# Performance work log

Hardware: AMD Instinct MI355X
Metric: run time of the kernel (lower is better)

The kernel has to match this reference:

```python
import jax, jax.numpy as jnp
import numpy as np

N_NODES = 50000
N_EDGES = 800000
F_IN = 512
HID = 256
N_CLS = 40
W_DIM = 50  # dimension*dimension*2 with dimension=5


def _prelu(x, a):
    return jnp.where(x >= 0, x, a * x)


def _segment_softmax(w, idx, n):
    # per-segment (grouped by idx), per-channel numerically stable softmax
    m = jax.ops.segment_max(w, idx, num_segments=n)
    e = jnp.exp(w - m[idx])
    s = jax.ops.segment_sum(e, idx, num_segments=n)
    return e / s[idx]


def _curvgn(x, edge_index, w_mul, W, b, w0, a, w1, b1):
    n = x.shape[0]
    h = x @ W + b                                   # [N, C]
    ow = _prelu(w_mul @ w0, a) @ w1 + b1            # [E, C] edge-weight MLP
    ow = _segment_softmax(ow, edge_index[0], n)     # softmax grouped by source (as in source)
    msg = ow * h[edge_index[0]]                     # gather x_j, weight
    return jax.ops.segment_sum(msg, edge_index[1], num_segments=n)  # scatter-add at target


def setup_inputs() -> dict:
    key = jax.random.key(0)
    ks = jax.random.split(key, 12)
    s = 0.05
    return {
        "x": jax.random.normal(ks[0], (N_NODES, F_IN), jnp.float32),
        "edge_index": jax.random.randint(ks[1], (2, N_EDGES), 0, N_NODES, jnp.int64 if jax.config.jax_enable_x64 else jnp.int32).astype(jnp.int32),
        "w_mul": jax.random.normal(ks[2], (N_EDGES, W_DIM), jnp.float32),
        "W1": jax.random.normal(ks[3], (F_IN, HID), jnp.float32) * s,
        "b1": jnp.zeros((HID,), jnp.float32),
        "m1_w0": jax.random.normal(ks[4], (W_DIM, HID), jnp.float32) * s,
        "m1_a": jnp.full((HID,), 0.2, jnp.float32),
        "m1_w1": jax.random.normal(ks[5], (HID, HID), jnp.float32) * s,
        "m1_b1": jnp.zeros((HID,), jnp.float32),
        "W2": jax.random.normal(ks[6], (HID, N_CLS), jnp.float32) * s,
        "b2": jnp.zeros((N_CLS,), jnp.float32),
        "m2_w0": jax.random.normal(ks[7], (W_DIM, N_CLS), jnp.float32) * s,
        "m2_a": jnp.full((N_CLS,), 0.2, jnp.float32),
        "m2_w1": jax.random.normal(ks[8], (N_CLS, N_CLS), jnp.float32) * s,
        "m2_b1": jnp.zeros((N_CLS,), jnp.float32),
    }


def reference(x, edge_index, w_mul, W1, b1, m1_w0, m1_a, m1_w1, m1_b1,
              W2, b2, m2_w0, m2_a, m2_w1, m2_b1):
    # eval mode: dropout is identity
    h = _curvgn(x, edge_index, w_mul, W1, b1, m1_w0, m1_a, m1_w1, m1_b1)
    h = jax.nn.elu(h)
    out = _curvgn(h, edge_index, w_mul, W2, b2, m2_w0, m2_a, m2_w1, m2_b1)
    return jax.nn.log_softmax(out, axis=1)
```

## Files before the change

### kernel.cpp

```cpp
#include <hip/hip_runtime.h>
#include <hip/hip_bf16.h>
#include <math.h>

#define N_NODESC 50000
#define N_EDGESC 800000
#define F_INC 512
#define HIDC 256
#define N_CLSC 40
#define W_DIMC 50
#define HN (2*N_NODESC)
#define NB_SCAN 196

typedef __bf16 bf16;
typedef __bf16 bf16x8 __attribute__((ext_vector_type(8)));
typedef __bf16 bf16x4 __attribute__((ext_vector_type(4)));
typedef __bf16 bf16x2 __attribute__((ext_vector_type(2)));
typedef float  f32x4  __attribute__((ext_vector_type(4)));
typedef float  f32x2  __attribute__((ext_vector_type(2)));

__global__ void k_hist(const int* __restrict__ ei, int* __restrict__ hist) {
    int e = blockIdx.x*256 + threadIdx.x;
    if (e < N_EDGESC) {
        atomicAdd(&hist[ei[e]], 1);
        atomicAdd(&hist[N_NODESC + ei[N_EDGESC + e]], 1);
    }
}
__global__ void k_copy(int* d, const int* s, int n) {
    int i = blockIdx.x*256 + threadIdx.x;
    if (i < n) d[i] = s[i];
}
__global__ void k_scan_part(const int* __restrict__ hist, int* __restrict__ part) {
    __shared__ int lds[512];
    int t = threadIdx.x;
    int i = blockIdx.x*512 + t;
    lds[t] = (i < HN) ? hist[i] : 0;
    __syncthreads();
    for (int off = 256; off > 0; off >>= 1) {
        if (t < off) lds[t] += lds[t+off];
        __syncthreads();
    }
    if (t == 0) part[blockIdx.x] = lds[0];
}
__global__ void k_scan_mid(const int* __restrict__ part, int* __restrict__ partx) {
    __shared__ int lds[256];
    int t = threadIdx.x;
    int v = (t < NB_SCAN) ? part[t] : 0;
    lds[t] = v;
    __syncthreads();
    for (int off = 1; off < 256; off <<= 1) {
        int add = (t >= off) ? lds[t-off] : 0;
        __syncthreads();
        lds[t] += add;
        __syncthreads();
    }
    partx[t] = lds[t] - v;
}
__global__ void k_scan_apply(const int* __restrict__ hist, const int* __restrict__ partx,
                             int* __restrict__ basev) {
    __shared__ int lds[512];
    int t = threadIdx.x;
    int i = blockIdx.x*512 + t;
    int v = (i < HN) ? hist[i] : 0;
    lds[t] = v;
    __syncthreads();
    for (int off = 1; off < 512; off <<= 1) {
        int add = (t >= off) ? lds[t-off] : 0;
        __syncthreads();
        lds[t] += add;
        __syncthreads();
    }
    if (i < HN) basev[i] = lds[t] - v + partx[blockIdx.x];
}
__global__ void k_scatter(const int* __restrict__ ei, int* __restrict__ cursor,
                          int* __restrict__ perm_src,
                          int* __restrict__ spd, int* __restrict__ svd) {
    int e = blockIdx.x*256 + threadIdx.x;
    if (e >= N_EDGESC) return;
    int s = ei[e];
    int d = ei[N_EDGESC + e];
    int p = atomicAdd(&cursor[s], 1);
    perm_src[p] = e;
    int q = atomicAdd(&cursor[N_NODESC + d], 1) - N_EDGESC;
    spd[q] = p;
    svd[q] = s;
}

__global__ void k_tconv(const float* __restrict__ src, bf16* __restrict__ dst,
                        int Ks, int Ns, int Kp, int Np) {
    int idx = blockIdx.x*256 + threadIdx.x;
    if (idx >= Kp*Np) return;
    int n = idx / Kp, k = idx - n*Kp;
    float v = (k < Ks && n < Ns) ? src[k*Ns + n] : 0.f;
    dst[idx] = (bf16)v;
}

__global__ __launch_bounds__(256) void k_h1(const float* __restrict__ x,
                                            const bf16* __restrict__ W1t,
                                            const float* __restrict__ b1,
                                            bf16* __restrict__ h1) {
    __shared__ __align__(16) bf16 a_lds[64*40];
    int tid = threadIdx.x;
    int lane = tid & 63, wv = tid >> 6;
    int l15 = lane & 15, quad = lane >> 4;
    int r0 = blockIdx.x * 64;
    f32x4 acc[4][4] = {};
    for (int ks = 0; ks < 16; ++ks) {
        #pragma unroll
        for (int i = 0; i < 2; ++i) {
            int idx = tid + i*256;
            int rl = idx >> 3, c4 = idx & 7;
            int rg = r0 + rl;
            f32x4 v = {};
            if (rg < N_NODESC) v = *(const f32x4*)&x[(size_t)rg*F_INC + ks*32 + c4*4];
            bf16x4 b; b[0]=(bf16)v[0]; b[1]=(bf16)v[1]; b[2]=(bf16)v[2]; b[3]=(bf16)v[3];
            *(bf16x4*)&a_lds[rl*40 + c4*4] = b;
        }
        __syncthreads();
        bf16x8 af[4], bfr[4];
        #pragma unroll
        for (int mt = 0; mt < 4; ++mt)
            af[mt] = *(const bf16x8*)&a_lds[(mt*16 + l15)*40 + quad*8];
        #pragma unroll
        for (int nt = 0; nt < 4; ++nt) {
            int n = wv*64 + nt*16 + l15;
            bfr[nt] = *(const bf16x8*)&W1t[n*F_INC + ks*32 + quad*8];
        }
        #pragma unroll
        for (int mt = 0; mt < 4; ++mt)
            #pragma unroll
            for (int nt = 0; nt < 4; ++nt)
                acc[mt][nt] = __builtin_amdgcn_mfma_f32_16x16x32_bf16(af[mt], bfr[nt], acc[mt][nt], 0, 0, 0);
        __syncthreads();
    }
    #pragma unroll
    for (int nt = 0; nt < 4; ++nt) {
        int col = wv*64 + nt*16 + l15;
        float bias = b1[col];
        #pragma unroll
        for (int mt = 0; mt < 4; ++mt)
            #pragma unroll
            for (int r = 0; r < 4; ++r) {
                int row = r0 + mt*16 + quad*4 + r;
                if (row < N_NODESC) h1[(size_t)row*HIDC + col] = (bf16)(acc[mt][nt][r] + bias);
            }
    }
}

__global__ __launch_bounds__(256) void k_mlp1a(
    const float* __restrict__ w_mul, const int* __restrict__ perm_src,
    const bf16* __restrict__ w0t, const float* __restrict__ a1,
    bf16* __restrict__ u1) {
    __shared__ __align__(16) bf16 wm[64*72];
    __shared__ __align__(16) bf16 bw[256*72];
    __shared__ int e_lds[64];
    int tid = threadIdx.x;
    int lane = tid & 63, wv = tid >> 6;
    int l15 = lane & 15, quad = lane >> 4;
    int p0 = blockIdx.x * 64;

    if (tid < 64) e_lds[tid] = perm_src[p0 + tid];
    #pragma unroll
    for (int i = 0; i < 8; ++i) {
        int idx = i*256 + tid;
        int n = idx >> 3, j = idx & 7;
        *(bf16x8*)&bw[n*72 + j*8] = *(const bf16x8*)&w0t[n*64 + j*8];
    }
    __syncthreads();
    #pragma unroll
    for (int i = 0; i < 7; ++i) {
        int idx = i*256 + tid;
        if (idx < 1600) {
            int row = idx / 25;
            int k = 2*(idx - row*25);
            f32x2 v = *(const f32x2*)&w_mul[(size_t)e_lds[row]*W_DIMC + k];
            bf16x2 b; b[0] = (bf16)v[0]; b[1] = (bf16)v[1];
            *(bf16x2*)&wm[row*72 + k] = b;
        }
    }
    #pragma unroll
    for (int i = 0; i < 2; ++i) {
        int idx = i*256 + tid;
        if (idx < 448) {
            int row = idx / 7, c = 50 + 2*(idx - row*7);
            bf16x2 z; z[0] = (bf16)0.f; z[1] = (bf16)0.f;
            *(bf16x2*)&wm[row*72 + c] = z;
        }
    }
    __syncthreads();

    f32x4 acc[4][4] = {};
    #pragma unroll
    for (int ks = 0; ks < 2; ++ks) {
        bf16x8 af[4], bfr[4];
        #pragma unroll
        for (int mt = 0; mt < 4; ++mt)
            af[mt] = *(const bf16x8*)&wm[(mt*16 + l15)*72 + ks*32 + quad*8];
        #pragma unroll
        for (int i = 0; i < 4; ++i)
            bfr[i] = *(const bf16x8*)&bw[(wv*64 + i*16 + l15)*72 + ks*32 + quad*8];
        #pragma unroll
        for (int mt = 0; mt < 4; ++mt)
            #pragma unroll
            for (int i = 0; i < 4; ++i)
                acc[mt][i] = __builtin_amdgcn_mfma_f32_16x16x32_bf16(af[mt], bfr[i], acc[mt][i], 0, 0, 0);
    }
    #pragma unroll
    for (int i = 0; i < 4; ++i) {
        int col = wv*64 + i*16 + l15;
        float al = a1[col];
        #pragma unroll
        for (int mt = 0; mt < 4; ++mt)
            #pragma unroll
            for (int r = 0; r < 4; ++r) {
                float v = acc[mt][i][r];
                v = (v >= 0.f) ? v : al*v;
                u1[(size_t)(p0 + mt*16 + quad*4 + r)*HIDC + col] = (bf16)v;
            }
    }
}

__global__ __launch_bounds__(256) void k_mlp1b(
    const int* __restrict__ perm_src, const int* __restrict__ ei,
    const bf16* __restrict__ w1t, const float* __restrict__ bb1,
    bf16* __restrict__ eow1,
    float* __restrict__ s1) {
    __shared__ __align__(16) bf16 t1[64*264];
    __shared__ int sv[64];
    int tid = threadIdx.x;
    int lane = tid & 63, wv = tid >> 6;
    int l15 = lane & 15, quad = lane >> 4;
    int p0 = blockIdx.x * 64;

    if (tid < 64) sv[tid] = ei[perm_src[p0 + tid]];
    #pragma unroll
    for (int i = 0; i < 8; ++i) {
        int idx = i*256 + tid;
        int row = idx >> 5, j = idx & 31;
        *(bf16x8*)&t1[row*264 + j*8] = *(const bf16x8*)&eow1[(size_t)(p0 + row)*HIDC + j*8];
    }
    __syncthreads();

    f32x4 acc[4][4] = {};
    #pragma unroll
    for (int ks = 0; ks < 8; ++ks) {
        bf16x8 af[4], bfr[4];
        #pragma unroll
        for (int mt = 0; mt < 4; ++mt)
            af[mt] = *(const bf16x8*)&t1[(mt*16 + l15)*264 + ks*32 + quad*8];
        #pragma unroll
        for (int i = 0; i < 4; ++i)
            bfr[i] = *(const bf16x8*)&w1t[(wv*64 + i*16 + l15)*HIDC + ks*32 + quad*8];
        #pragma unroll
        for (int mt = 0; mt < 4; ++mt)
            #pragma unroll
            for (int i = 0; i < 4; ++i)
                acc[mt][i] = __builtin_amdgcn_mfma_f32_16x16x32_bf16(af[mt], bfr[i], acc[mt][i], 0, 0, 0);
    }
    __syncthreads();
    #pragma unroll
    for (int i = 0; i < 4; ++i) {
        int col = wv*64 + i*16 + l15;
        float bias = bb1[col];
        #pragma unroll
        for (int mt = 0; mt < 4; ++mt)
            #pragma unroll
            for (int r = 0; r < 4; ++r)
                t1[(mt*16 + quad*4 + r)*264 + col] = (bf16)__expf(acc[mt][i][r] + bias);
    }
    __syncthreads();
    #pragma unroll
    for (int i = 0; i < 8; ++i) {
        int idx = i*256 + tid;
        int row = idx >> 5, j = idx & 31;
        *(bf16x8*)&eow1[(size_t)(p0 + row)*HIDC + j*8] = *(const bf16x8*)&t1[row*264 + j*8];
    }
    {
        int c = tid;
        float acc2 = 0.f;
        #pragma unroll
        for (int r = 0; r < 64; ++r) {
            acc2 += (float)t1[r*264 + c];
            if (r == 63 || sv[r+1] != sv[r]) {
                atomicAdd(&s1[(size_t)sv[r]*HIDC + c], acc2);
                acc2 = 0.f;
            }
        }
    }
}

__global__ __launch_bounds__(256) void k_mlp2(
    const float* __restrict__ w_mul, const int* __restrict__ perm_src,
    const int* __restrict__ ei,
    const bf16* __restrict__ w20t, const float* __restrict__ a2,
    const bf16* __restrict__ w21t, const float* __restrict__ bb2,
    bf16* __restrict__ eow2, float* __restrict__ s2) {
    __shared__ __align__(16) bf16 wm[64*72];
    __shared__ __align__(16) bf16 t2[64*72];
    __shared__ int e_lds[64], sv[64];
    int tid = threadIdx.x;
    int lane = tid & 63, wv = tid >> 6;
    int l15 = lane & 15, quad = lane >> 4;
    int p0 = blockIdx.x * 64;

    if (tid < 64) {
        int e = perm_src[p0 + tid];
        e_lds[tid] = e;
        sv[tid] = ei[e];
    }
    __syncthreads();
    #pragma unroll
    for (int i = 0; i < 7; ++i) {
        int idx = i*256 + tid;
        if (idx < 1600) {
            int row = idx / 25;
            int k = 2*(idx - row*25);
            f32x2 v = *(const f32x2*)&w_mul[(size_t)e_lds[row]*W_DIMC + k];
            bf16x2 b; b[0] = (bf16)v[0]; b[1] = (bf16)v[1];
            *(bf16x2*)&wm[row*72 + k] = b;
        }
    }
    #pragma unroll
    for (int i = 0; i < 2; ++i) {
        int idx = i*256 + tid;
        if (idx < 448) {
            int row = idx / 7, c = 50 + 2*(idx - row*7);
            bf16x2 z; z[0] = (bf16)0.f; z[1] = (bf16)0.f;
            *(bf16x2*)&wm[row*72 + c] = z;
        }
    }
    #pragma unroll
    for (int i = 0; i < 2; ++i) {
        int idx = i*256 + tid;
        int row = idx >> 3, c = 48 + 2*(idx & 7);
        bf16x2 z; z[0] = (bf16)0.f; z[1] = (bf16)0.f;
        *(bf16x2*)&t2[row*72 + c] = z;
    }
    __syncthreads();

    {
        f32x4 acc[3] = {};
        #pragma unroll
        for (int ks = 0; ks < 2; ++ks) {
            bf16x8 af = *(const bf16x8*)&wm[(wv*16 + l15)*72 + ks*32 + quad*8];
            #pragma unroll
            for (int i = 0; i < 3; ++i) {
                bf16x8 bfr = *(const bf16x8*)&w20t[(i*16 + l15)*64 + ks*32 + quad*8];
                acc[i] = __builtin_amdgcn_mfma_f32_16x16x32_bf16(af, bfr, acc[i], 0, 0, 0);
            }
        }
        #pragma unroll
        for (int i = 0; i < 3; ++i) {
            int col = i*16 + l15;
            float al = (col < N_CLSC) ? a2[col] : 0.f;
            #pragma unroll
            for (int r = 0; r < 4; ++r) {
                float v = acc[i][r];
                v = (v >= 0.f) ? v : al*v;
                t2[(wv*16 + quad*4 + r)*72 + col] = (bf16)v;
            }
        }
    }
    __syncthreads();
    {
        f32x4 acc[3] = {};
        #pragma unroll
        for (int ks = 0; ks < 2; ++ks) {
            bf16x8 af = *(const bf16x8*)&t2[(wv*16 + l15)*72 + ks*32 + quad*8];
            #pragma unroll
            for (int i = 0; i < 3; ++i) {
                bf16x8 bfr = *(const bf16x8*)&w21t[(i*16 + l15)*64 + ks*32 + quad*8];
                acc[i] = __builtin_amdgcn_mfma_f32_16x16x32_bf16(af, bfr, acc[i], 0, 0, 0);
            }
        }
        __syncthreads();
        #pragma unroll
        for (int i = 0; i < 3; ++i) {
            int col = i*16 + l15;
            if (col < N_CLSC) {
                float bias = bb2[col];
                #pragma unroll
                for (int r = 0; r < 4; ++r)
                    t2[(wv*16 + quad*4 + r)*72 + col] = (bf16)__expf(acc[i][r] + bias);
            }
        }
    }
    __syncthreads();
    #pragma unroll
    for (int i = 0; i < 2; ++i) {
        int idx = i*256 + tid;
        if (idx < 320) {
            int row = idx / 5, c8 = idx % 5;
            bf16x8 v = *(const bf16x8*)&t2[row*72 + c8*8];
            *(bf16x8*)&eow2[(size_t)(p0 + row)*N_CLSC + c8*8] = v;
        }
    }
    if (tid < 240) {
        int c = tid % 40, g = tid / 40;
        int rA = g*11, rB = (rA + 11 < 64) ? rA + 11 : 64;
        float acc = 0.f;
        for (int r = rA; r < rB; ++r) {
            acc += (float)t2[r*72 + c];
            if (r == rB-1 || sv[r+1] != sv[r]) {
                atomicAdd(&s2[(size_t)sv[r]*N_CLSC + c], acc);
                acc = 0.f;
            }
        }
    }
}

__global__ __launch_bounds__(256) void k_agg1(
    const bf16* __restrict__ eow1, const bf16* __restrict__ g1,
    const int* __restrict__ basev, const int* __restrict__ spd,
    const int* __restrict__ svd, float* __restrict__ out1) {
    int v = blockIdx.x, c = threadIdx.x;
    int b = basev[N_NODESC + v] - N_EDGESC;
    int e = (v < N_NODESC-1) ? basev[N_NODESC + v + 1] - N_EDGESC : N_EDGESC;
    float acc = 0.f;
    #pragma unroll 2
    for (int j = b; j < e; ++j) {
        int sp = spd[j], s = svd[j];
        acc += (float)eow1[(size_t)sp*HIDC + c] * (float)g1[(size_t)s*HIDC + c];
    }
    out1[(size_t)v*HIDC + c] = (acc > 0.f) ? acc : expm1f(acc);
}

__global__ __launch_bounds__(64) void k_agg2(
    const bf16* __restrict__ eow2, const bf16* __restrict__ g2,
    const int* __restrict__ basev, const int* __restrict__ spd,
    const int* __restrict__ svd, float* __restrict__ out) {
    int v = blockIdx.x, c = threadIdx.x;
    int b = basev[N_NODESC + v] - N_EDGESC;
    int e = (v < N_NODESC-1) ? basev[N_NODESC + v + 1] - N_EDGESC : N_EDGESC;
    bool act = (c < N_CLSC);
    float acc = 0.f;
    #pragma unroll 2
    for (int j = b; j < e; ++j) {
        int sp = spd[j], s = svd[j];
        if (act) acc += (float)eow2[(size_t)sp*N_CLSC + c] * (float)g2[(size_t)s*N_CLSC + c];
    }
    float m = act ? acc : -INFINITY;
    #pragma unroll
    for (int off = 32; off > 0; off >>= 1) m = fmaxf(m, __shfl_xor(m, off));
    float ex = act ? __expf(acc - m) : 0.f;
    #pragma unroll
    for (int off = 32; off > 0; off >>= 1) ex += __shfl_xor(ex, off);
    if (act) out[(size_t)v*N_CLSC + c] = acc - m - logf(ex);
}

__global__ void k_div_bf4(bf16* __restrict__ h, const float* __restrict__ s, int n4) {
    int i = blockIdx.x*256 + threadIdx.x;
    if (i < n4) {
        bf16x4 hv = *(bf16x4*)&h[i*4];
        f32x4 sv = *(const f32x4*)&s[i*4];
        #pragma unroll
        for (int k = 0; k < 4; ++k) hv[k] = (bf16)((float)hv[k] / sv[k]);
        *(bf16x4*)&h[i*4] = hv;
    }
}
__global__ void k_h2(const float* __restrict__ out1, const float* __restrict__ W2,
                     const float* __restrict__ b2, bf16* __restrict__ h2) {
    int i = blockIdx.x*256 + threadIdx.x;
    if (i >= N_NODESC*N_CLSC) return;
    int v = i / N_CLSC, c = i - v*N_CLSC;
    float acc = b2[c];
    const float* row = &out1[(size_t)v*HIDC];
    #pragma unroll 4
    for (int k = 0; k < HIDC; ++k) acc += row[k] * W2[k*N_CLSC + c];
    h2[i] = (bf16)acc;
}

extern "C" void kernel_launch(void* const* d_in, const int* in_sizes, int n_in,
                              void* d_out, int out_size, void* d_ws, size_t ws_size,
                              hipStream_t stream) {
    const float* x    = (const float*)d_in[0];
    const int*   ei   = (const int*)d_in[1];
    const float* wmul = (const float*)d_in[2];
    const float* W1   = (const float*)d_in[3];
    const float* b1   = (const float*)d_in[4];
    const float* m1w0 = (const float*)d_in[5];
    const float* m1a  = (const float*)d_in[6];
    const float* m1w1 = (const float*)d_in[7];
    const float* m1b1 = (const float*)d_in[8];
    const float* W2   = (const float*)d_in[9];
    const float* b2   = (const float*)d_in[10];
    const float* m2w0 = (const float*)d_in[11];
    const float* m2a  = (const float*)d_in[12];
    const float* m2w1 = (const float*)d_in[13];
    const float* m2b1 = (const float*)d_in[14];
    float* out = (float*)d_out;

    char* ws = (char*)d_ws;
    size_t off = 0;
    auto alloc = [&](size_t bytes) -> void* {
        off = (off + 255) & ~(size_t)255;
        void* p = ws + off;
        off += bytes;
        return p;
    };
    bf16*  h1g1  = (bf16*) alloc((size_t)N_NODESC*HIDC*2);
    float* s1o1  = (float*)alloc((size_t)N_NODESC*HIDC*4);
    bf16*  h2g2  = (bf16*) alloc((size_t)N_NODESC*N_CLSC*2);
    float* s2    = (float*)alloc((size_t)N_NODESC*N_CLSC*4);
    bf16*  W1t   = (bf16*) alloc(256*512*2);
    bf16*  w0t   = (bf16*) alloc(256*64*2);
    bf16*  w1tm  = (bf16*) alloc(256*256*2);
    bf16*  w20t  = (bf16*) alloc(48*64*2);
    bf16*  w21t  = (bf16*) alloc(48*64*2);
    int*   hist  = (int*)  alloc(HN*4);
    int*   basev = (int*)  alloc(HN*4);
    int*   cursor= (int*)  alloc(HN*4);
    int*   part  = (int*)  alloc(256*4);
    int*   partx = (int*)  alloc(256*4);
    int*   perm_src = (int*)alloc((size_t)N_EDGESC*4);
    int*   spd      = (int*)alloc((size_t)N_EDGESC*4);
    int*   svd      = (int*)alloc((size_t)N_EDGESC*4);
    bf16*  eow1  = (bf16*) alloc((size_t)N_EDGESC*HIDC*2);
    bf16*  eow2  = (bf16*) alloc((size_t)N_EDGESC*N_CLSC*2);

    hipMemsetAsync(hist, 0, HN*4, stream);
    hipMemsetAsync(s1o1, 0, (size_t)N_NODESC*HIDC*4, stream);
    hipMemsetAsync(s2,   0, (size_t)N_NODESC*N_CLSC*4, stream);
    k_hist<<<(N_EDGESC+255)/256, 256, 0, stream>>>(ei, hist);
    k_scan_part<<<NB_SCAN, 512, 0, stream>>>(hist, part);
    k_scan_mid<<<1, 256, 0, stream>>>(part, partx);
    k_scan_apply<<<NB_SCAN, 512, 0, stream>>>(hist, partx, basev);
    k_copy<<<(HN+255)/256, 256, 0, stream>>>(cursor, basev, HN);
    k_scatter<<<(N_EDGESC+255)/256, 256, 0, stream>>>(ei, cursor, perm_src, spd, svd);

    k_tconv<<<(512*256+255)/256, 256, 0, stream>>>(W1,   W1t, 512, 256, 512, 256);
    k_tconv<<<(256*64+255)/256,  256, 0, stream>>>(m1w0, w0t,  50, 256,  64, 256);
    k_tconv<<<(256*256+255)/256, 256, 0, stream>>>(m1w1, w1tm, 256, 256, 256, 256);
    k_tconv<<<(48*64+255)/256,   256, 0, stream>>>(m2w0, w20t,  50,  40,  64,  48);
    k_tconv<<<(48*64+255)/256,   256, 0, stream>>>(m2w1, w21t,  40,  40,  64,  48);

    k_h1<<<(N_NODESC+63)/64, 256, 0, stream>>>(x, W1t, b1, h1g1);
    k_mlp1a<<<N_EDGESC/64, 256, 0, stream>>>(wmul, perm_src, w0t, m1a, eow1);
    k_mlp1b<<<N_EDGESC/64, 256, 0, stream>>>(perm_src, ei, w1tm, m1b1, eow1, s1o1);
    k_mlp2<<<N_EDGESC/64, 256, 0, stream>>>(wmul, perm_src, ei, w20t, m2a, w21t, m2b1,
                                            eow2, s2);
    k_div_bf4<<<(N_NODESC*HIDC/4+255)/256, 256, 0, stream>>>(h1g1, s1o1, N_NODESC*HIDC/4);
    k_agg1<<<N_NODESC, 256, 0, stream>>>(eow1, h1g1, basev, spd, svd, s1o1);

    k_h2<<<(N_NODESC*N_CLSC+255)/256, 256, 0, stream>>>(s1o1, W2, b2, h2g2);
    k_div_bf4<<<(N_NODESC*N_CLSC/4+255)/256, 256, 0, stream>>>(h2g2, s2, N_NODESC*N_CLSC/4);
    k_agg2<<<N_NODESC, 64, 0, stream>>>(eow2, h2g2, basev, spd, svd, out);
}
```

Baseline: 1.745 ms.

## Fuse layer-1 edge MLP kernels and double edge tile in layer-2 MLP

Merges the two layer-1 edge-MLP kernels into one, so the PReLU intermediate stays in shared memory rather than being written to and re-read from the global eow1 buffer. The second GEMM now double-buffers its operand fragments across k-steps, and the first reads w0t directly from global memory instead of staging it in LDS. The layer-2 edge MLP handles 128 edges per block, with each wave computing two M-tiles, and one barrier between its stages is dropped. This cuts global traffic and launch count, at the cost of higher register pressure and a different shared-memory footprint and occupancy.

New measurement: 1.501 ms. 14.0% less time.

```diff
diff --git a/kernel.cpp b/kernel.cpp
--- a/kernel.cpp
+++ b/kernel.cpp
@@ -146,24 +146,24 @@
     }
 }
 
-__global__ __launch_bounds__(256) void k_mlp1a(
+__global__ __launch_bounds__(256) void k_mlp1(
     const float* __restrict__ w_mul, const int* __restrict__ perm_src,
+    const int* __restrict__ ei,
     const bf16* __restrict__ w0t, const float* __restrict__ a1,
-    bf16* __restrict__ u1) {
+    const bf16* __restrict__ w1t, const float* __restrict__ bb1,
+    bf16* __restrict__ eow1, float* __restrict__ s1) {
     __shared__ __align__(16) bf16 wm[64*72];
-    __shared__ __align__(16) bf16 bw[256*72];
-    __shared__ int e_lds[64];
+    __shared__ __align__(16) bf16 t1[64*264];
+    __shared__ int e_lds[64], sv[64];
     int tid = threadIdx.x;
     int lane = tid & 63, wv = tid >> 6;
     int l15 = lane & 15, quad = lane >> 4;
     int p0 = blockIdx.x * 64;
 
-    if (tid < 64) e_lds[tid] = perm_src[p0 + tid];
-    #pragma unroll
-    for (int i = 0; i < 8; ++i) {
-        int idx = i*256 + tid;
-        int n = idx >> 3, j = idx & 7;
-        *(bf16x8*)&bw[n*72 + j*8] = *(const bf16x8*)&w0t[n*64 + j*8];
+    if (tid < 64) {
+        int e = perm_src[p0 + tid];
+        e_lds[tid] = e;
+        sv[tid] = ei[e];
     }
     __syncthreads();
     #pragma unroll
@@ -188,86 +188,81 @@
     }
     __syncthreads();
 
-    f32x4 acc[4][4] = {};
-    #pragma unroll
-    for (int ks = 0; ks < 2; ++ks) {
-        bf16x8 af[4], bfr[4];
+    {
+        f32x4 acc[4][4] = {};
+        bf16x8 af[2][4], bfr[2][4];
+        #pragma unroll
+        for (int ks = 0; ks < 2; ++ks) {
+            #pragma unroll
+            for (int mt = 0; mt < 4; ++mt)
+                af[ks][mt] = *(const bf16x8*)&wm[(mt*16 + l15)*72 + ks*32 + quad*8];
+            #pragma unroll
+            for (int i = 0; i < 4; ++i)
+                bfr[ks][i] = *(const bf16x8*)&w0t[(wv*64 + i*16 + l15)*64 + ks*32 + quad*8];
+        }
+        #pragma unroll
+        for (int ks = 0; ks < 2; ++ks)
+            #pragma unroll
+            for (int mt = 0; mt < 4; ++mt)
+                #pragma unroll
+                for (int i = 0; i < 4; ++i)
+                    acc[mt][i] = __builtin_amdgcn_mfma_f32_16x16x32_bf16(af[ks][mt], bfr[ks][i], acc[mt][i], 0, 0, 0);
+        #pragma unroll
+        for (int i = 0; i < 4; ++i) {
+            int col = wv*64 + i*16 + l15;
+            float al = a1[col];
+            #pragma unroll
+            for (int mt = 0; mt < 4; ++mt)
+                #pragma unroll
+                for (int r = 0; r < 4; ++r) {
+                    float v = acc[mt][i][r];
+                    v = (v >= 0.f) ? v : al*v;
+                    t1[(mt*16 + quad*4 + r)*264 + col] = (bf16)v;
+                }
+        }
+    }
+    __syncthreads();
+
+    {
+        f32x4 acc[4][4] = {};
+        bf16x8 af[2][4], bfr[2][4];
         #pragma unroll
         for (int mt = 0; mt < 4; ++mt)
-            af[mt] = *(const bf16x8*)&wm[(mt*16 + l15)*72 + ks*32 + quad*8];
+            af[0][mt] = *(const bf16x8*)&t1[(mt*16 + l15)*264 + quad*8];
         #pragma unroll
         for (int i = 0; i < 4; ++i)
-            bfr[i] = *(const bf16x8*)&bw[(wv*64 + i*16 + l15)*72 + ks*32 + quad*8];
-        #pragma unroll
-        for (int mt = 0; mt < 4; ++mt)
-            #pragma unroll
-            for (int i = 0; i < 4; ++i)
-                acc[mt][i] = __builtin_amdgcn_mfma_f32_16x16x32_bf16(af[mt], bfr[i], acc[mt][i], 0, 0, 0);
-    }
-    #pragma unroll
-    for (int i = 0; i < 4; ++i) {
-        int col = wv*64 + i*16 + l15;
-        float al = a1[col];
-        #pragma unroll
-        for (int mt = 0; mt < 4; ++mt)
-            #pragma unroll
-            for (int r = 0; r < 4; ++r) {
-                float v = acc[mt][i][r];
-                v = (v >= 0.f) ? v : al*v;
-                u1[(size_t)(p0 + mt*16 + quad*4 + r)*HIDC + col] = (bf16)v;
+            bfr[0][i] = *(const bf16x8*)&w1t[(wv*64 + i*16 + l15)*HIDC + quad*8];
+        #pragma unroll
+        for (int ks = 0; ks < 8; ++ks) {
+            int cur = ks & 1, nxt = cur ^ 1;
+            if (ks < 7) {
+                #pragma unroll
+                for (int mt = 0; mt < 4; ++mt)
+                    af[nxt][mt] = *(const bf16x8*)&t1[(mt*16 + l15)*264 + (ks+1)*32 + quad*8];
+                #pragma unroll
+                for (int i = 0; i < 4; ++i)
+                    bfr[nxt][i] = *(const bf16x8*)&w1t[(wv*64 + i*16 + l15)*HIDC + (ks+1)*32 + quad*8];
             }
-    }
-}
-
-__global__ __launch_bounds__(256) void k_mlp1b(
-    const int* __restrict__ perm_src, const int* __restrict__ ei,
-    const bf16* __restrict__ w1t, const float* __restrict__ bb1,
-    bf16* __restrict__ eow1,
-    float* __restrict__ s1) {
-    __shared__ __align__(16) bf16 t1[64*264];
-    __shared__ int sv[64];
-    int tid = threadIdx.x;
-    int lane = tid & 63, wv = tid >> 6;
-    int l15 = lane & 15, quad = lane >> 4;
-    int p0 = blockIdx.x * 64;
-
-    if (tid < 64) sv[tid] = ei[perm_src[p0 + tid]];
-    #pragma unroll
-    for (int i = 0; i < 8; ++i) {
-        int idx = i*256 + tid;
-        int row = idx >> 5, j = idx & 31;
-        *(bf16x8*)&t1[row*264 + j*8] = *(const bf16x8*)&eow1[(size_t)(p0 + row)*HIDC + j*8];
-    }
-    __syncthreads();
-
-    f32x4 acc[4][4] = {};
-    #pragma unroll
-    for (int ks = 0; ks < 8; ++ks) {
-        bf16x8 af[4], bfr[4];
-        #pragma unroll
-        for (int mt = 0; mt < 4; ++mt)
-            af[mt] = *(const bf16x8*)&t1[(mt*16 + l15)*264 + ks*32 + quad*8];
-        #pragma unroll
-        for (int i = 0; i < 4; ++i)
-            bfr[i] = *(const bf16x8*)&w1t[(wv*64 + i*16 + l15)*HIDC + ks*32 + quad*8];
-        #pragma unroll
-        for (int mt = 0; mt < 4; ++mt)
-            #pragma unroll
-            for (int i = 0; i < 4; ++i)
-                acc[mt][i] = __builtin_amdgcn_mfma_f32_16x16x32_bf16(af[mt], bfr[i], acc[mt][i], 0, 0, 0);
-    }
-    __syncthreads();
-    #pragma unroll
-    for (int i = 0; i < 4; ++i) {
-        int col = wv*64 + i*16 + l15;
-        float bias = bb1[col];
-        #pragma unroll
-        for (int mt = 0; mt < 4; ++mt)
-            #pragma unroll
-            for (int r = 0; r < 4; ++r)
-                t1[(mt*16 + quad*4 + r)*264 + col] = (bf16)__expf(acc[mt][i][r] + bias);
-    }
-    __syncthreads();
+            #pragma unroll
+            for (int mt = 0; mt < 4; ++mt)
+                #pragma unroll
+                for (int i = 0; i < 4; ++i)
+                    acc[mt][i] = __builtin_amdgcn_mfma_f32_16x16x32_bf16(af[cur][mt], bfr[cur][i], acc[mt][i], 0, 0, 0);
+        }
+        __syncthreads();
+        #pragma unroll
+        for (int i = 0; i < 4; ++i) {
+            int col = wv*64 + i*16 + l15;
+            float bias = bb1[col];
+            #pragma unroll
+            for (int mt = 0; mt < 4; ++mt)
+                #pragma unroll
+                for (int r = 0; r < 4; ++r)
+                    t1[(mt*16 + quad*4 + r)*264 + col] = (bf16)__expf(acc[mt][i][r] + bias);
+        }
+    }
+    __syncthreads();
+
     #pragma unroll
     for (int i = 0; i < 8; ++i) {
         int idx = i*256 + tid;
@@ -294,24 +289,24 @@
     const bf16* __restrict__ w20t, const float* __restrict__ a2,
     const bf16* __restrict__ w21t, const float* __restrict__ bb2,
     bf16* __restrict__ eow2, float* __restrict__ s2) {
-    __shared__ __align__(16) bf16 wm[64*72];
-    __shared__ __align__(16) bf16 t2[64*72];
-    __shared__ int e_lds[64], sv[64];
+    __shared__ __align__(16) bf16 wm[128*72];
+    __shared__ __align__(16) bf16 t2[128*72];
+    __shared__ int e_lds[128], sv[128];
     int tid = threadIdx.x;
     int lane = tid & 63, wv = tid >> 6;
     int l15 = lane & 15, quad = lane >> 4;
-    int p0 = blockIdx.x * 64;
-
-    if (tid < 64) {
+    int p0 = blockIdx.x * 128;
+
+    if (tid < 128) {
         int e = perm_src[p0 + tid];
         e_lds[tid] = e;
         sv[tid] = ei[e];
     }
     __syncthreads();
     #pragma unroll
-    for (int i = 0; i < 7; ++i) {
-        int idx = i*256 + tid;
-        if (idx < 1600) {
+    for (int i = 0; i < 13; ++i) {
+        int idx = i*256 + tid;
+        if (idx < 3200) {
             int row = idx / 25;
             int k = 2*(idx - row*25);
             f32x2 v = *(const f32x2*)&w_mul[(size_t)e_lds[row]*W_DIMC + k];
@@ -320,16 +315,16 @@
         }
     }
     #pragma unroll
-    for (int i = 0; i < 2; ++i) {
-        int idx = i*256 + tid;
-        if (idx < 448) {
+    for (int i = 0; i < 4; ++i) {
+        int idx = i*256 + tid;
+        if (idx < 896) {
             int row = idx / 7, c = 50 + 2*(idx - row*7);
             bf16x2 z; z[0] = (bf16)0.f; z[1] = (bf16)0.f;
             *(bf16x2*)&wm[row*72 + c] = z;
         }
     }
     #pragma unroll
-    for (int i = 0; i < 2; ++i) {
+    for (int i = 0; i < 4; ++i) {
         int idx = i*256 + tid;
         int row = idx >> 3, c = 48 + 2*(idx & 7);
         bf16x2 z; z[0] = (bf16)0.f; z[1] = (bf16)0.f;
@@ -338,57 +333,73 @@
     __syncthreads();
 
     {
-        f32x4 acc[3] = {};
+        f32x4 acc[2][3] = {};
         #pragma unroll
         for (int ks = 0; ks < 2; ++ks) {
-            bf16x8 af = *(const bf16x8*)&wm[(wv*16 + l15)*72 + ks*32 + quad*8];
-            #pragma unroll
-            for (int i = 0; i < 3; ++i) {
-                bf16x8 bfr = *(const bf16x8*)&w20t[(i*16 + l15)*64 + ks*32 + quad*8];
-                acc[i] = __builtin_amdgcn_mfma_f32_16x16x32_bf16(af, bfr, acc[i], 0, 0, 0);
-            }
+            bf16x8 af[2], bfr[3];
+            #pragma unroll
+            for (int mt = 0; mt < 2; ++mt)
+                af[mt] = *(const bf16x8*)&wm[(wv*32 + mt*16 + l15)*72 + ks*32 + quad*8];
+            #pragma unroll
+            for (int i = 0; i < 3; ++i)
+                bfr[i] = *(const bf16x8*)&w20t[(i*16 + l15)*64 + ks*32 + quad*8];
+            #pragma unroll
+            for (int mt = 0; mt < 2; ++mt)
+                #pragma unroll
+                for (int i = 0; i < 3; ++i)
+                    acc[mt][i] = __builtin_amdgcn_mfma_f32_16x16x32_bf16(af[mt], bfr[i], acc[mt][i], 0, 0, 0);
         }
         #pragma unroll
         for (int i = 0; i < 3; ++i) {
             int col = i*16 + l15;
             float al = (col < N_CLSC) ? a2[col] : 0.f;
             #pragma unroll
-            for (int r = 0; r < 4; ++r) {
-                float v = acc[i][r];
-                v = (v >= 0.f) ? v : al*v;
-                t2[(wv*16 + quad*4 + r)*72 + col] = (bf16)v;
-            }
-        }
-    }
-    __syncthreads();
+            for (int mt = 0; mt < 2; ++mt)
+                #pragma unroll
+                for (int r = 0; r < 4; ++r) {
+                    float v = acc[mt][i][r];
+                    v = (v >= 0.f) ? v : al*v;
+                    t2[(wv*32 + mt*16 + quad*4 + r)*72 + col] = (bf16)v;
+                }
+        }
+    }
+
     {
-        f32x4 acc[3] = {};
+        f32x4 acc[2][3] = {};
         #pragma unroll
         for (int ks = 0; ks < 2; ++ks) {
-            bf16x8 af = *(const bf16x8*)&t2[(wv*16 + l15)*72 + ks*32 + quad*8];
-            #pragma unroll
-            for (int i = 0; i < 3; ++i) {
-                bf16x8 bfr = *(const bf16x8*)&w21t[(i*16 + l15)*64 + ks*32 + quad*8];
-                acc[i] = __builtin_amdgcn_mfma_f32_16x16x32_bf16(af, bfr, acc[i], 0, 0, 0);
-            }
-        }
-        __syncthreads();
+            bf16x8 af[2], bfr[3];
+            #pragma unroll
+            for (int mt = 0; mt < 2; ++mt)
+                af[mt] = *(const bf16x8*)&t2[(wv*32 + mt*16 + l15)*72 + ks*32 + quad*8];
+            #pragma unroll
+            for (int i = 0; i < 3; ++i)
+                bfr[i] = *(const bf16x8*)&w21t[(i*16 + l15)*64 + ks*32 + quad*8];
+            #pragma unroll
+            for (int mt = 0; mt < 2; ++mt)
+                #pragma unroll
+                for (int i = 0; i < 3; ++i)
+                    acc[mt][i] = __builtin_amdgcn_mfma_f32_16x16x32_bf16(af[mt], bfr[i], acc[mt][i], 0, 0, 0);
+        }
         #pragma unroll
         for (int i = 0; i < 3; ++i) {
             int col = i*16 + l15;
             if (col < N_CLSC) {
                 float bias = bb2[col];
                 #pragma unroll
-                for (int r = 0; r < 4; ++r)
-                    t2[(wv*16 + quad*4 + r)*72 + col] = (bf16)__expf(acc[i][r] + bias);
+                for (int mt = 0; mt < 2; ++mt)
+                    #pragma unroll
+                    for (int r = 0; r < 4; ++r)
+                        t2[(wv*32 + mt*16 + quad*4 + r)*72 + col] = (bf16)__expf(acc[mt][i][r] + bias);
             }
         }
     }
     __syncthreads();
-    #pragma unroll
-    for (int i = 0; i < 2; ++i) {
-        int idx = i*256 + tid;
-        if (idx < 320) {
+
+    #pragma unroll
+    for (int i = 0; i < 3; ++i) {
+        int idx = i*256 + tid;
+        if (idx < 640) {
             int row = idx / 5, c8 = idx % 5;
             bf16x8 v = *(const bf16x8*)&t2[row*72 + c8*8];
             *(bf16x8*)&eow2[(size_t)(p0 + row)*N_CLSC + c8*8] = v;
@@ -396,7 +407,7 @@
     }
     if (tid < 240) {
         int c = tid % 40, g = tid / 40;
-        int rA = g*11, rB = (rA + 11 < 64) ? rA + 11 : 64;
+        int rA = g*22, rB = (rA + 22 < 128) ? rA + 22 : 128;
         float acc = 0.f;
         for (int r = rA; r < rB; ++r) {
             acc += (float)t2[r*72 + c];
@@ -534,10 +545,10 @@
     k_tconv<<<(48*64+255)/256,   256, 0, stream>>>(m2w1, w21t,  40,  40,  64,  48);
 
     k_h1<<<(N_NODESC+63)/64, 256, 0, stream>>>(x, W1t, b1, h1g1);
-    k_mlp1a<<<N_EDGESC/64, 256, 0, stream>>>(wmul, perm_src, w0t, m1a, eow1);
-    k_mlp1b<<<N_EDGESC/64, 256, 0, stream>>>(perm_src, ei, w1tm, m1b1, eow1, s1o1);
-    k_mlp2<<<N_EDGESC/64, 256, 0, stream>>>(wmul, perm_src, ei, w20t, m2a, w21t, m2b1,
-                                            eow2, s2);
+    k_mlp1<<<N_EDGESC/64, 256, 0, stream>>>(wmul, perm_src, ei, w0t, m1a, w1tm, m1b1,
+                                            eow1, s1o1);
+    k_mlp2<<<N_EDGESC/128, 256, 0, stream>>>(wmul, perm_src, ei, w20t, m2a, w21t, m2b1,
+                                             eow2, s2);
     k_div_bf4<<<(N_NODESC*HIDC/4+255)/256, 256, 0, stream>>>(h1g1, s1o1, N_NODESC*HIDC/4);
     k_agg1<<<N_NODESC, 256, 0, stream>>>(eow1, h1g1, basev, spd, svd, s1o1);
 
```
